# Optimization experiments

Hardware: AMD Instinct MI355X
Metric: run time of the kernel (lower is better)

## Reference

```python
import jax, jax.numpy as jnp
import numpy as np

E, K, N, T, TOPK, GROUP_SIZE = 8, 2048, 2048, 1024, 2, 128


def setup_inputs() -> dict:
    key = jax.random.key(0)
    ks = jax.random.split(key, 6)
    x = jax.random.normal(ks[0], (T, K), dtype=jnp.float32)
    # uint8-quantized weights stored as int32 (values 0..255)
    w_q = jax.random.randint(ks[1], (E, K, N), 0, 256, dtype=jnp.int32)
    scales = jax.random.uniform(ks[2], (E, K, K // GROUP_SIZE), dtype=jnp.float32) * 0.02
    zeros = jax.random.normal(ks[3], (E, K, K // GROUP_SIZE), dtype=jnp.float32) * 0.1
    topk_weights = jax.random.uniform(ks[4], (T, TOPK), dtype=jnp.float32)
    topk_ids = jax.random.randint(ks[5], (T, TOPK), 0, E, dtype=jnp.int32)
    return {"x": x, "w_q": w_q, "scales": scales, "zeros": zeros,
            "topk_weights": topk_weights, "topk_ids": topk_ids}


def reference(x, w_q, scales, zeros, topk_weights, topk_ids):
    # Faithful to _moe_kernel_w8a16: for each (token, expert-slot) pair,
    #   out[t, n] += topk_weight * sum_k x[t, k] * (w_q[e, k, n] * scales[e, k, k//gs] + zeros[e, k, k//gs])
    # Note the kernel broadcasts scale/zero over n (offs_n * 0) with group index k // group_size.
    k_idx = jnp.arange(K)
    g_idx = k_idx // GROUP_SIZE                      # (K,)
    s = scales[:, k_idx, g_idx]                       # (E, K) scale per (e, k)
    z = zeros[:, k_idx, g_idx]                        # (E, K)
    w_deq = w_q.astype(jnp.float32) * s[:, :, None] + z[:, :, None]  # (E, K, N)
    # dense per-expert GEMM, then gather the top_k experts per token
    all_out = jnp.einsum('tk,ekn->ten', x, w_deq)     # (T, E, N)
    sel = jnp.take_along_axis(all_out, topk_ids[:, :, None].astype(jnp.int32), axis=1)  # (T, TOPK, N)
    out = jnp.sum(sel * topk_weights[:, :, None], axis=1)  # (T, N)
    return out
```

## Files before the change

### kernel.cpp

```cpp
#include <hip/hip_runtime.h>
#include <hip/hip_bf16.h>
#include <stdint.h>

#define E_    8
#define K_    2048
#define N_    2048
#define T_    1024
#define TOPK_ 2
#define NG_   16
#define MAXM  512

#define BM 128
#define BN 64
#define BK 64
#define NST (K_ / BK)
#define MTILES (MAXM / BM)

typedef __attribute__((ext_vector_type(8))) short bf16x8;
typedef __attribute__((ext_vector_type(4))) float f32x4;
typedef __attribute__((ext_vector_type(4))) unsigned int u32x4;
typedef __attribute__((ext_vector_type(8))) unsigned short u16x8;

__device__ __forceinline__ unsigned short f2bf_rne(float f) {
    unsigned u = __float_as_uint(f);
    u += 0x7fffu + ((u >> 16) & 1u);
    return (unsigned short)(u >> 16);
}
__device__ __forceinline__ unsigned short f2bf_trunc(float f) {
    return (unsigned short)(__float_as_uint(f) >> 16);
}

__device__ __forceinline__ void gload_lds16(const void* g, void* l) {
    __builtin_amdgcn_global_load_lds(
        (__attribute__((address_space(1))) unsigned int*)g,
        (__attribute__((address_space(3))) unsigned int*)l,
        16, 0, 0);
}

__global__ void prep_sz(const float* __restrict__ scales, const float* __restrict__ zeros,
                        float* __restrict__ sd, float* __restrict__ zd, int* __restrict__ cnt)
{
    int i = blockIdx.x * 256 + threadIdx.x;
    int e = i >> 11;
    int k = i & (K_ - 1);
    int g = k >> 7;
    size_t src = ((size_t)e * K_ + k) * NG_ + g;
    sd[i] = scales[src];
    zd[i] = zeros[src];
    if (i < E_) cnt[i] = 0;
}

__global__ void route_k(const int* __restrict__ topk_ids, int* __restrict__ cnt,
                        int* __restrict__ ptj)
{
    int idx = blockIdx.x * 256 + threadIdx.x;
    if (idx < T_ * TOPK_) {
        int e = topk_ids[idx];
        int slot = atomicAdd(&cnt[e], 1);
        if (slot < T_ * TOPK_) ptj[e * (T_ * TOPK_) + slot] = idx;
    }
}

__global__ void zdot_k(const float* __restrict__ x, const float* __restrict__ zdiag,
                       const int* __restrict__ topk_ids, float* __restrict__ zdot)
{
    int w = (int)((blockIdx.x * blockDim.x + threadIdx.x) >> 6);
    int lane = threadIdx.x & 63;
    int t = w >> 1;
    int e = topk_ids[w];
    const f32x4* xp = (const f32x4*)(x + (size_t)t * K_);
    const f32x4* zp = (const f32x4*)(zdiag + (size_t)e * K_);
    float acc = 0.f;
#pragma unroll
    for (int it = 0; it < K_ / 256; ++it) {
        f32x4 a = xp[it * 64 + lane];
        f32x4 b = zp[it * 64 + lane];
        acc += a.x * b.x + a.y * b.y + a.z * b.z + a.w * b.w;
    }
#pragma unroll
    for (int off = 32; off > 0; off >>= 1) acc += __shfl_xor(acc, off);
    if (lane == 0) zdot[w] = acc;
}

__global__ void aprep_k(const float* __restrict__ x, const float* __restrict__ sdiag,
                        const int* __restrict__ cnt, const int* __restrict__ ptj,
                        unsigned short* __restrict__ apack)
{
    int e = blockIdx.y;
    int slot = blockIdx.x;
    if (slot >= min(cnt[e], MAXM)) return;
    int tj = ptj[e * (T_ * TOPK_) + slot];
    int t = tj >> 1;
    const float* xr = x + (size_t)t * K_;
    const float* sr = sdiag + (size_t)e * K_;
    int k = threadIdx.x * 8;
    f32x4 a0 = *(const f32x4*)(xr + k);
    f32x4 s0 = *(const f32x4*)(sr + k);
    f32x4 a1 = *(const f32x4*)(xr + k + 4);
    f32x4 s1 = *(const f32x4*)(sr + k + 4);
    u16x8 h;
    h[0] = f2bf_rne(a0.x * s0.x);
    h[1] = f2bf_rne(a0.y * s0.y);
    h[2] = f2bf_rne(a0.z * s0.z);
    h[3] = f2bf_rne(a0.w * s0.w);
    h[4] = f2bf_rne(a1.x * s1.x);
    h[5] = f2bf_rne(a1.y * s1.y);
    h[6] = f2bf_rne(a1.z * s1.z);
    h[7] = f2bf_rne(a1.w * s1.w);
    *(u16x8*)(apack + ((size_t)e * MAXM + slot) * K_ + k) = h;
}

__global__ __launch_bounds__(256, 3)
void moe_gemm(const int* __restrict__ wq, const unsigned short* __restrict__ apack,
              const float* __restrict__ topk_w, const int* __restrict__ cnt,
              const int* __restrict__ ptj, const float* __restrict__ zdot,
              float* __restrict__ part, float* __restrict__ out, int use_part)
{
    int e = blockIdx.z;
    int count = min(cnt[e], MAXM);
    int m0 = blockIdx.y * BM;
    if (m0 >= count) return;
    int n0 = blockIdx.x * BN;

    __shared__ alignas(16) unsigned short As[2][BM * BK];
    __shared__ alignas(16) unsigned short Bs[2][BN * BK];

    int tid = threadIdx.x;
    int lane = tid & 63;
    int wid = tid >> 6;
    int wm = (wid >> 1) * 64;
    int wn = (wid & 1) * 32;

    int lrow = lane >> 3;
    int lcol = lane & 7;
    int aswz = (lcol ^ lrow) << 4;
    const char* abase = (const char*)(apack + (size_t)e * MAXM * K_);

    int b_n = tid & 63;
    int b_set = tid >> 6;
    const int* wcol = wq + (size_t)e * K_ * N_ + n0 + b_n;
    int bswz = (b_n & 7) << 4;

    f32x4 acc[4][2] = {};
    int b0[16], b1[16], b2[16];

    auto stageA = [&](int buf, int kt) {
        int kk = kt * BK;
#pragma unroll
        for (int ci = 0; ci < 4; ++ci) {
            int c = wid * 4 + ci;
            int p = m0 + c * 8 + lrow;
            const char* g = abase + ((size_t)p * K_ + kk) * 2 + aswz;
            gload_lds16(g, (char*)As[buf] + c * 1024);
        }
    };
    auto loadB = [&](int* br, int kt) {
        int kb = kt * BK + b_set * 16;
#pragma unroll
        for (int i = 0; i < 16; ++i)
            br[i] = wcol[(kb + i) * N_];
    };
    auto packB = [&](const int* br, int buf) {
        unsigned pk[8];
#pragma unroll
        for (int i = 0; i < 8; ++i) {
            unsigned lo = f2bf_trunc((float)br[2 * i]);
            unsigned hi = f2bf_trunc((float)br[2 * i + 1]);
            pk[i] = lo | (hi << 16);
        }
        char* bsrow = (char*)Bs[buf] + b_n * (BK * 2);
#pragma unroll
        for (int seg = 0; seg < 2; ++seg) {
            int kbyte = b_set * 32 + seg * 16;
            u32x4 v = { pk[seg * 4], pk[seg * 4 + 1], pk[seg * 4 + 2], pk[seg * 4 + 3] };
            *(u32x4*)(bsrow + (kbyte ^ bswz)) = v;
        }
    };
    auto comp = [&](int buf) {
#pragma unroll
        for (int kk2 = 0; kk2 < 2; ++kk2) {
            int kb = kk2 * 64 + ((lane >> 4) << 4);
            bf16x8 af[4], bfr[2];
#pragma unroll
            for (int mi = 0; mi < 4; ++mi) {
                int row = wm + mi * 16 + (lane & 15);
                af[mi] = *(const bf16x8*)((const char*)As[buf] + row * 128 + (kb ^ ((row & 7) << 4)));
            }
#pragma unroll
            for (int ni = 0; ni < 2; ++ni) {
                int row = wn + ni * 16 + (lane & 15);
                bfr[ni] = *(const bf16x8*)((const char*)Bs[buf] + row * 128 + (kb ^ ((row & 7) << 4)));
            }
#pragma unroll
            for (int mi = 0; mi < 4; ++mi)
#pragma unroll
                for (int ni = 0; ni < 2; ++ni)
                    acc[mi][ni] = __builtin_amdgcn_mfma_f32_16x16x32_bf16(
                        af[mi], bfr[ni], acc[mi][ni], 0, 0, 0);
        }
    };

    stageA(0, 0);
    __builtin_amdgcn_sched_barrier(0);
    loadB(b0, 0);
    loadB(b1, 1);
    loadB(b2, 2);
    packB(b0, 0);
    asm volatile("s_waitcnt vmcnt(32) lgkmcnt(0)" ::: "memory");
    __builtin_amdgcn_s_barrier();
    __builtin_amdgcn_sched_barrier(0);

    int kt = 0;
#define STEP(C, BL, BP) do {                                                  \
        stageA(C ^ 1, kt + 1);                                                \
        __builtin_amdgcn_sched_barrier(0);                                    \
        loadB(BL, kt + 3);                                                    \
        comp(C);                                                              \
        packB(BP, C ^ 1);                                                     \
        asm volatile("s_waitcnt vmcnt(16) lgkmcnt(0)" ::: "memory");          \
        __builtin_amdgcn_s_barrier();                                         \
        __builtin_amdgcn_sched_barrier(0);                                    \
        ++kt;                                                                 \
    } while (0)

#pragma unroll 1
    for (int it = 0; it < 4; ++it) {
        STEP(0, b0, b1);
        STEP(1, b1, b2);
        STEP(0, b2, b0);
        STEP(1, b0, b1);
        STEP(0, b1, b2);
        STEP(1, b2, b0);
    }
    STEP(0, b0, b1);
    STEP(1, b1, b2);
    STEP(0, b2, b0);
    STEP(1, b0, b1);
    STEP(0, b1, b2);
#undef STEP
    stageA(0, 30);
    __builtin_amdgcn_sched_barrier(0);
    comp(1);
    packB(b0, 0);
    asm volatile("s_waitcnt vmcnt(0) lgkmcnt(0)" ::: "memory");
    __builtin_amdgcn_s_barrier();
    __builtin_amdgcn_sched_barrier(0);
    stageA(1, 31);
    __builtin_amdgcn_sched_barrier(0);
    comp(0);
    packB(b1, 1);
    asm volatile("s_waitcnt vmcnt(0) lgkmcnt(0)" ::: "memory");
    __builtin_amdgcn_s_barrier();
    __builtin_amdgcn_sched_barrier(0);
    comp(1);

#pragma unroll
    for (int mi = 0; mi < 4; ++mi) {
        int prow = m0 + wm + mi * 16 + ((lane >> 4) << 2);
#pragma unroll
        for (int r = 0; r < 4; ++r) {
            int p = prow + r;
            if (p < count) {
                int tj = ptj[e * (T_ * TOPK_) + p];
                float w = topk_w[tj];
                float zdv = zdot[tj];
                float v0 = w * (acc[mi][0][r] + zdv);
                float v1 = w * (acc[mi][1][r] + zdv);
                if (use_part) {
                    float* pr = part + (size_t)tj * N_ + n0 + wn + (lane & 15);
                    pr[0]  = v0;
                    pr[16] = v1;
                } else {
                    float* orow = out + (size_t)(tj >> 1) * N_ + n0 + wn + (lane & 15);
                    atomicAdd(orow + 0,  v0);
                    atomicAdd(orow + 16, v1);
                }
            }
        }
    }
}

__global__ void reduce_k(const float* __restrict__ part, float* __restrict__ out)
{
    int g = blockIdx.x * 256 + threadIdx.x;
    int t = g >> 9;
    int nc = g & 511;
    f32x4 a = ((const f32x4*)part)[((size_t)(t * 2) << 9) + nc];
    f32x4 b = ((const f32x4*)part)[((size_t)(t * 2 + 1) << 9) + nc];
    ((f32x4*)out)[g] = a + b;
}

extern "C" void kernel_launch(void* const* d_in, const int* in_sizes, int n_in,
                              void* d_out, int out_size, void* d_ws, size_t ws_size,
                              hipStream_t stream)
{
    const float* x       = (const float*)d_in[0];
    const int*   wq      = (const int*)d_in[1];
    const float* scales  = (const float*)d_in[2];
    const float* zeros   = (const float*)d_in[3];
    const float* topk_w  = (const float*)d_in[4];
    const int*   topk_id = (const int*)d_in[5];
    float* out = (float*)d_out;

    char* ws = (char*)d_ws;
    float* sdiag = (float*)(ws + 0);
    float* zdiag = (float*)(ws + 65536);
    int*   cnt   = (int*)(ws + 131072);
    int*   ptj   = (int*)(ws + 135168);
    float* zdot  = (float*)(ws + 200704);
    unsigned short* apack = (unsigned short*)(ws + (1 << 20));
    float* part  = (float*)(ws + ((size_t)17 << 20));
    size_t need = ((size_t)17 << 20) + (size_t)T_ * TOPK_ * N_ * sizeof(float);
    int use_part = (ws_size >= need) ? 1 : 0;

    prep_sz<<<E_ * K_ / 256, 256, 0, stream>>>(scales, zeros, sdiag, zdiag, cnt);
    route_k<<<T_ * TOPK_ / 256, 256, 0, stream>>>(topk_id, cnt, ptj);
    zdot_k<<<T_ * TOPK_ / 4, 256, 0, stream>>>(x, zdiag, topk_id, zdot);
    aprep_k<<<dim3(MAXM, E_), 256, 0, stream>>>(x, sdiag, cnt, ptj, apack);
    if (!use_part)
        hipMemsetAsync(d_out, 0, (size_t)T_ * N_ * sizeof(float), stream);
    moe_gemm<<<dim3(N_ / BN, MTILES, E_), 256, 0, stream>>>(
        wq, apack, topk_w, cnt, ptj, zdot, part, out, use_part);
    if (use_part)
        reduce_k<<<T_ * N_ / 4 / 256, 256, 0, stream>>>(part, out);
}
```

Before: 83.41 us.

## Triple-buffer A tile in LDS to prefetch two k-steps ahead

Adds a third LDS buffer for the activation tile so the direct-to-LDS A loads are issued two k-steps ahead instead of one. The A and B buffer indices are decoupled in the compute routine, and the wait counts are relaxed so more global loads stay in flight. The extra LDS use comes with dropping the occupancy hint from 3 to 2 blocks per CU, which trades latency hiding across blocks for deeper prefetch within a block.

```diff
diff --git a/kernel.cpp b/kernel.cpp
--- a/kernel.cpp
+++ b/kernel.cpp
@@ -110,7 +110,7 @@
     *(u16x8*)(apack + ((size_t)e * MAXM + slot) * K_ + k) = h;
 }
 
-__global__ __launch_bounds__(256, 3)
+__global__ __launch_bounds__(256, 2)
 void moe_gemm(const int* __restrict__ wq, const unsigned short* __restrict__ apack,
               const float* __restrict__ topk_w, const int* __restrict__ cnt,
               const int* __restrict__ ptj, const float* __restrict__ zdot,
@@ -122,7 +122,7 @@
     if (m0 >= count) return;
     int n0 = blockIdx.x * BN;
 
-    __shared__ alignas(16) unsigned short As[2][BM * BK];
+    __shared__ alignas(16) unsigned short As[3][BM * BK];
     __shared__ alignas(16) unsigned short Bs[2][BN * BK];
 
     int tid = threadIdx.x;
@@ -160,7 +160,7 @@
         for (int i = 0; i < 16; ++i)
             br[i] = wcol[(kb + i) * N_];
     };
-    auto packB = [&](const int* br, int buf) {
+    auto packB = [&](const int* br, int bbuf) {
         unsigned pk[8];
 #pragma unroll
         for (int i = 0; i < 8; ++i) {
@@ -168,7 +168,7 @@
             unsigned hi = f2bf_trunc((float)br[2 * i + 1]);
             pk[i] = lo | (hi << 16);
         }
-        char* bsrow = (char*)Bs[buf] + b_n * (BK * 2);
+        char* bsrow = (char*)Bs[bbuf] + b_n * (BK * 2);
 #pragma unroll
         for (int seg = 0; seg < 2; ++seg) {
             int kbyte = b_set * 32 + seg * 16;
@@ -176,7 +176,7 @@
             *(u32x4*)(bsrow + (kbyte ^ bswz)) = v;
         }
     };
-    auto comp = [&](int buf) {
+    auto comp = [&](int abuf, int bbuf) {
 #pragma unroll
         for (int kk2 = 0; kk2 < 2; ++kk2) {
             int kb = kk2 * 64 + ((lane >> 4) << 4);
@@ -184,12 +184,12 @@
 #pragma unroll
             for (int mi = 0; mi < 4; ++mi) {
                 int row = wm + mi * 16 + (lane & 15);
-                af[mi] = *(const bf16x8*)((const char*)As[buf] + row * 128 + (kb ^ ((row & 7) << 4)));
+                af[mi] = *(const bf16x8*)((const char*)As[abuf] + row * 128 + (kb ^ ((row & 7) << 4)));
             }
 #pragma unroll
             for (int ni = 0; ni < 2; ++ni) {
                 int row = wn + ni * 16 + (lane & 15);
-                bfr[ni] = *(const bf16x8*)((const char*)Bs[buf] + row * 128 + (kb ^ ((row & 7) << 4)));
+                bfr[ni] = *(const bf16x8*)((const char*)Bs[bbuf] + row * 128 + (kb ^ ((row & 7) << 4)));
             }
 #pragma unroll
             for (int mi = 0; mi < 4; ++mi)
@@ -201,6 +201,7 @@
     };
 
     stageA(0, 0);
+    stageA(1, 1);
     __builtin_amdgcn_sched_barrier(0);
     loadB(b0, 0);
     loadB(b1, 1);
@@ -211,13 +212,13 @@
     __builtin_amdgcn_sched_barrier(0);
 
     int kt = 0;
-#define STEP(C, BL, BP) do {                                                  \
-        stageA(C ^ 1, kt + 1);                                                \
+#define STEP(CA, SA, BL, BP, CB, PB) do {                                     \
+        stageA(SA, kt + 2);                                                   \
         __builtin_amdgcn_sched_barrier(0);                                    \
         loadB(BL, kt + 3);                                                    \
-        comp(C);                                                              \
-        packB(BP, C ^ 1);                                                     \
-        asm volatile("s_waitcnt vmcnt(16) lgkmcnt(0)" ::: "memory");          \
+        comp(CA, CB);                                                         \
+        packB(BP, PB);                                                        \
+        asm volatile("s_waitcnt vmcnt(36) lgkmcnt(0)" ::: "memory");          \
         __builtin_amdgcn_s_barrier();                                         \
         __builtin_amdgcn_sched_barrier(0);                                    \
         ++kt;                                                                 \
@@ -225,34 +226,32 @@
 
 #pragma unroll 1
     for (int it = 0; it < 4; ++it) {
-        STEP(0, b0, b1);
-        STEP(1, b1, b2);
-        STEP(0, b2, b0);
-        STEP(1, b0, b1);
-        STEP(0, b1, b2);
-        STEP(1, b2, b0);
+        STEP(0, 2, b0, b1, 0, 1);
+        STEP(1, 0, b1, b2, 1, 0);
+        STEP(2, 1, b2, b0, 0, 1);
+        STEP(0, 2, b0, b1, 1, 0);
+        STEP(1, 0, b1, b2, 0, 1);
+        STEP(2, 1, b2, b0, 1, 0);
     }
-    STEP(0, b0, b1);
-    STEP(1, b1, b2);
-    STEP(0, b2, b0);
-    STEP(1, b0, b1);
-    STEP(0, b1, b2);
+    STEP(0, 2, b0, b1, 0, 1);
+    STEP(1, 0, b1, b2, 1, 0);
+    STEP(2, 1, b2, b0, 0, 1);
+    STEP(0, 2, b0, b1, 1, 0);
+    STEP(1, 0, b1, b2, 0, 1);
 #undef STEP
-    stageA(0, 30);
-    __builtin_amdgcn_sched_barrier(0);
-    comp(1);
+    stageA(1, 31);
+    __builtin_amdgcn_sched_barrier(0);
+    comp(2, 1);
     packB(b0, 0);
-    asm volatile("s_waitcnt vmcnt(0) lgkmcnt(0)" ::: "memory");
+    asm volatile("s_waitcnt vmcnt(20) lgkmcnt(0)" ::: "memory");
     __builtin_amdgcn_s_barrier();
     __builtin_amdgcn_sched_barrier(0);
-    stageA(1, 31);
-    __builtin_amdgcn_sched_barrier(0);
-    comp(0);
+    comp(0, 0);
     packB(b1, 1);
     asm volatile("s_waitcnt vmcnt(0) lgkmcnt(0)" ::: "memory");
     __builtin_amdgcn_s_barrier();
     __builtin_amdgcn_sched_barrier(0);
-    comp(1);
+    comp(1, 1);
 
 #pragma unroll
     for (int mi = 0; mi < 4; ++mi) {
```

After: 104.6 us. 1.25x slower.

## Stage A tiles through registers instead of direct global-to-LDS loads

Applied to the files above, without the earlier changes.

Replaces the global_load_lds path for activation tiles with plain vector register loads, two k-steps ahead, followed by swizzled LDS writes after compute. The pipeline is restructured into a uniform 30-step loop and the explicit vmcnt waits and sched_barriers are dropped, leaving vmem waits to the compiler. This gives the compiler more freedom to schedule, at the cost of extra VGPRs for A prefetch and extra LDS write instructions. Loop bounds also change, with B loads clamped at the last tile and redundant loads in the final steps.

```diff
diff --git a/kernel.cpp b/kernel.cpp
--- a/kernel.cpp
+++ b/kernel.cpp
@@ -18,6 +18,7 @@
 
 typedef __attribute__((ext_vector_type(8))) short bf16x8;
 typedef __attribute__((ext_vector_type(4))) float f32x4;
+typedef __attribute__((ext_vector_type(4))) int i32x4;
 typedef __attribute__((ext_vector_type(4))) unsigned int u32x4;
 typedef __attribute__((ext_vector_type(8))) unsigned short u16x8;
 
@@ -28,13 +29,6 @@
 }
 __device__ __forceinline__ unsigned short f2bf_trunc(float f) {
     return (unsigned short)(__float_as_uint(f) >> 16);
-}
-
-__device__ __forceinline__ void gload_lds16(const void* g, void* l) {
-    __builtin_amdgcn_global_load_lds(
-        (__attribute__((address_space(1))) unsigned int*)g,
-        (__attribute__((address_space(3))) unsigned int*)l,
-        16, 0, 0);
 }
 
 __global__ void prep_sz(const float* __restrict__ scales, const float* __restrict__ zeros,
@@ -131,10 +125,11 @@
     int wm = (wid >> 1) * 64;
     int wn = (wid & 1) * 32;
 
-    int lrow = lane >> 3;
-    int lcol = lane & 7;
-    int aswz = (lcol ^ lrow) << 4;
-    const char* abase = (const char*)(apack + (size_t)e * MAXM * K_);
+    int arow = tid >> 3;
+    int asl = tid & 7;
+    const char* ag = (const char*)(apack + (size_t)e * MAXM * K_)
+                   + ((size_t)(m0 + arow) * K_) * 2 + asl * 16;
+    int alds = arow * 128 + ((asl ^ (arow & 7)) << 4);
 
     int b_n = tid & 63;
     int b_set = tid >> 6;
@@ -142,17 +137,20 @@
     int bswz = (b_n & 7) << 4;
 
     f32x4 acc[4][2] = {};
+    i32x4 a0[4], a1[4];
     int b0[16], b1[16], b2[16];
 
-    auto stageA = [&](int buf, int kt) {
-        int kk = kt * BK;
-#pragma unroll
-        for (int ci = 0; ci < 4; ++ci) {
-            int c = wid * 4 + ci;
-            int p = m0 + c * 8 + lrow;
-            const char* g = abase + ((size_t)p * K_ + kk) * 2 + aswz;
-            gload_lds16(g, (char*)As[buf] + c * 1024);
-        }
+    auto loadA = [&](i32x4* dst, int kt) {
+        const char* base = ag + (size_t)kt * (BK * 2);
+#pragma unroll
+        for (int r = 0; r < 4; ++r)
+            dst[r] = *(const i32x4*)(base + (size_t)r * 32 * K_ * 2);
+    };
+    auto writeA = [&](const i32x4* src, int abuf) {
+        char* l = (char*)As[abuf] + alds;
+#pragma unroll
+        for (int r = 0; r < 4; ++r)
+            *(u32x4*)(l + r * 4096) = __builtin_bit_cast(u32x4, src[r]);
     };
     auto loadB = [&](int* br, int kt) {
         int kb = kt * BK + b_set * 16;
@@ -160,7 +158,7 @@
         for (int i = 0; i < 16; ++i)
             br[i] = wcol[(kb + i) * N_];
     };
-    auto packB = [&](const int* br, int buf) {
+    auto packB = [&](const int* br, int bbuf) {
         unsigned pk[8];
 #pragma unroll
         for (int i = 0; i < 8; ++i) {
@@ -168,7 +166,7 @@
             unsigned hi = f2bf_trunc((float)br[2 * i + 1]);
             pk[i] = lo | (hi << 16);
         }
-        char* bsrow = (char*)Bs[buf] + b_n * (BK * 2);
+        char* bsrow = (char*)Bs[bbuf] + b_n * (BK * 2);
 #pragma unroll
         for (int seg = 0; seg < 2; ++seg) {
             int kbyte = b_set * 32 + seg * 16;
@@ -200,58 +198,46 @@
         }
     };
 
-    stageA(0, 0);
-    __builtin_amdgcn_sched_barrier(0);
+    loadA(a0, 0);
+    loadA(a1, 1);
     loadB(b0, 0);
     loadB(b1, 1);
     loadB(b2, 2);
+    writeA(a0, 0);
     packB(b0, 0);
-    asm volatile("s_waitcnt vmcnt(32) lgkmcnt(0)" ::: "memory");
+    asm volatile("s_waitcnt lgkmcnt(0)" ::: "memory");
     __builtin_amdgcn_s_barrier();
-    __builtin_amdgcn_sched_barrier(0);
+    asm volatile("" ::: "memory");
 
     int kt = 0;
-#define STEP(C, BL, BP) do {                                                  \
-        stageA(C ^ 1, kt + 1);                                                \
-        __builtin_amdgcn_sched_barrier(0);                                    \
-        loadB(BL, kt + 3);                                                    \
-        comp(C);                                                              \
-        packB(BP, C ^ 1);                                                     \
-        asm volatile("s_waitcnt vmcnt(16) lgkmcnt(0)" ::: "memory");          \
+#define STEP(AL, BL, CC, AW, BP) do {                                         \
+        loadA(AL, kt + 2);                                                    \
+        loadB(BL, min(kt + 3, NST - 1));                                      \
+        comp(CC);                                                             \
+        writeA(AW, CC ^ 1);                                                   \
+        packB(BP, CC ^ 1);                                                    \
+        asm volatile("s_waitcnt lgkmcnt(0)" ::: "memory");                    \
         __builtin_amdgcn_s_barrier();                                         \
-        __builtin_amdgcn_sched_barrier(0);                                    \
+        asm volatile("" ::: "memory");                                        \
         ++kt;                                                                 \
     } while (0)
 
 #pragma unroll 1
-    for (int it = 0; it < 4; ++it) {
-        STEP(0, b0, b1);
-        STEP(1, b1, b2);
-        STEP(0, b2, b0);
-        STEP(1, b0, b1);
-        STEP(0, b1, b2);
-        STEP(1, b2, b0);
+    for (int it = 0; it < 5; ++it) {
+        STEP(a0, b0, 0, a1, b1);
+        STEP(a1, b1, 1, a0, b2);
+        STEP(a0, b2, 0, a1, b0);
+        STEP(a1, b0, 1, a0, b1);
+        STEP(a0, b1, 0, a1, b2);
+        STEP(a1, b2, 1, a0, b0);
     }
-    STEP(0, b0, b1);
-    STEP(1, b1, b2);
-    STEP(0, b2, b0);
-    STEP(1, b0, b1);
-    STEP(0, b1, b2);
 #undef STEP
-    stageA(0, 30);
-    __builtin_amdgcn_sched_barrier(0);
-    comp(1);
-    packB(b0, 0);
-    asm volatile("s_waitcnt vmcnt(0) lgkmcnt(0)" ::: "memory");
+    comp(0);
+    writeA(a1, 1);
+    packB(b1, 1);
+    asm volatile("s_waitcnt lgkmcnt(0)" ::: "memory");
     __builtin_amdgcn_s_barrier();
-    __builtin_amdgcn_sched_barrier(0);
-    stageA(1, 31);
-    __builtin_amdgcn_sched_barrier(0);
-    comp(0);
-    packB(b1, 1);
-    asm volatile("s_waitcnt vmcnt(0) lgkmcnt(0)" ::: "memory");
-    __builtin_amdgcn_s_barrier();
-    __builtin_amdgcn_sched_barrier(0);
+    asm volatile("" ::: "memory");
     comp(1);
 
 #pragma unroll
```

Result: slower. 90.14 us (+8.1%).

## Double GEMM M-tile to 256 with 512 threads and fuse zero-dot into aprep

Applied to the files above, without the earlier changes.

Raises the GEMM block M-tile from 128 to 256 rows and launches 512 threads per block, so each block reuses every loaded weight column for twice as many tokens. The B loading is redistributed so each thread loads 8 k-rows instead of 16, with the waitcnt values adjusted to match. Separately, the zero-point dot product is computed inside aprep_k, removing one kernel launch and a second read of x. Trade-offs: fewer blocks in flight (MTILES halves) and more shared memory per block, which may reduce occupancy and load balance across experts.

```diff
diff --git a/kernel.cpp b/kernel.cpp
--- a/kernel.cpp
+++ b/kernel.cpp
@@ -10,7 +10,7 @@
 #define NG_   16
 #define MAXM  512
 
-#define BM 128
+#define BM 256
 #define BN 64
 #define BK 64
 #define NST (K_ / BK)
@@ -61,30 +61,10 @@
     }
 }
 
-__global__ void zdot_k(const float* __restrict__ x, const float* __restrict__ zdiag,
-                       const int* __restrict__ topk_ids, float* __restrict__ zdot)
-{
-    int w = (int)((blockIdx.x * blockDim.x + threadIdx.x) >> 6);
-    int lane = threadIdx.x & 63;
-    int t = w >> 1;
-    int e = topk_ids[w];
-    const f32x4* xp = (const f32x4*)(x + (size_t)t * K_);
-    const f32x4* zp = (const f32x4*)(zdiag + (size_t)e * K_);
-    float acc = 0.f;
-#pragma unroll
-    for (int it = 0; it < K_ / 256; ++it) {
-        f32x4 a = xp[it * 64 + lane];
-        f32x4 b = zp[it * 64 + lane];
-        acc += a.x * b.x + a.y * b.y + a.z * b.z + a.w * b.w;
-    }
-#pragma unroll
-    for (int off = 32; off > 0; off >>= 1) acc += __shfl_xor(acc, off);
-    if (lane == 0) zdot[w] = acc;
-}
-
 __global__ void aprep_k(const float* __restrict__ x, const float* __restrict__ sdiag,
+                        const float* __restrict__ zdiag,
                         const int* __restrict__ cnt, const int* __restrict__ ptj,
-                        unsigned short* __restrict__ apack)
+                        unsigned short* __restrict__ apack, float* __restrict__ zdot)
 {
     int e = blockIdx.y;
     int slot = blockIdx.x;
@@ -93,11 +73,14 @@
     int t = tj >> 1;
     const float* xr = x + (size_t)t * K_;
     const float* sr = sdiag + (size_t)e * K_;
+    const float* zr = zdiag + (size_t)e * K_;
     int k = threadIdx.x * 8;
     f32x4 a0 = *(const f32x4*)(xr + k);
     f32x4 s0 = *(const f32x4*)(sr + k);
     f32x4 a1 = *(const f32x4*)(xr + k + 4);
     f32x4 s1 = *(const f32x4*)(sr + k + 4);
+    f32x4 z0 = *(const f32x4*)(zr + k);
+    f32x4 z1 = *(const f32x4*)(zr + k + 4);
     u16x8 h;
     h[0] = f2bf_rne(a0.x * s0.x);
     h[1] = f2bf_rne(a0.y * s0.y);
@@ -108,9 +91,20 @@
     h[6] = f2bf_rne(a1.z * s1.z);
     h[7] = f2bf_rne(a1.w * s1.w);
     *(u16x8*)(apack + ((size_t)e * MAXM + slot) * K_ + k) = h;
-}
-
-__global__ __launch_bounds__(256, 3)
+    float zp = a0.x * z0.x + a0.y * z0.y + a0.z * z0.z + a0.w * z0.w
+             + a1.x * z1.x + a1.y * z1.y + a1.z * z1.z + a1.w * z1.w;
+#pragma unroll
+    for (int off = 32; off > 0; off >>= 1) zp += __shfl_down(zp, off);
+    __shared__ float red[4];
+    int lane = threadIdx.x & 63;
+    int w = threadIdx.x >> 6;
+    if (lane == 0) red[w] = zp;
+    __syncthreads();
+    if (threadIdx.x == 0)
+        zdot[tj] = red[0] + red[1] + red[2] + red[3];
+}
+
+__global__ __launch_bounds__(512, 2)
 void moe_gemm(const int* __restrict__ wq, const unsigned short* __restrict__ apack,
               const float* __restrict__ topk_w, const int* __restrict__ cnt,
               const int* __restrict__ ptj, const float* __restrict__ zdot,
@@ -137,12 +131,12 @@
     const char* abase = (const char*)(apack + (size_t)e * MAXM * K_);
 
     int b_n = tid & 63;
-    int b_set = tid >> 6;
+    int b_kq = tid >> 6;
     const int* wcol = wq + (size_t)e * K_ * N_ + n0 + b_n;
     int bswz = (b_n & 7) << 4;
 
     f32x4 acc[4][2] = {};
-    int b0[16], b1[16], b2[16];
+    int b0[8], b1[8], b2[8];
 
     auto stageA = [&](int buf, int kt) {
         int kk = kt * BK;
@@ -155,26 +149,23 @@
         }
     };
     auto loadB = [&](int* br, int kt) {
-        int kb = kt * BK + b_set * 16;
-#pragma unroll
-        for (int i = 0; i < 16; ++i)
+        int kb = kt * BK + b_kq * 8;
+#pragma unroll
+        for (int i = 0; i < 8; ++i)
             br[i] = wcol[(kb + i) * N_];
     };
-    auto packB = [&](const int* br, int buf) {
-        unsigned pk[8];
-#pragma unroll
-        for (int i = 0; i < 8; ++i) {
+    auto packB = [&](const int* br, int bbuf) {
+        unsigned pk[4];
+#pragma unroll
+        for (int i = 0; i < 4; ++i) {
             unsigned lo = f2bf_trunc((float)br[2 * i]);
             unsigned hi = f2bf_trunc((float)br[2 * i + 1]);
             pk[i] = lo | (hi << 16);
         }
-        char* bsrow = (char*)Bs[buf] + b_n * (BK * 2);
-#pragma unroll
-        for (int seg = 0; seg < 2; ++seg) {
-            int kbyte = b_set * 32 + seg * 16;
-            u32x4 v = { pk[seg * 4], pk[seg * 4 + 1], pk[seg * 4 + 2], pk[seg * 4 + 3] };
-            *(u32x4*)(bsrow + (kbyte ^ bswz)) = v;
-        }
+        char* bsrow = (char*)Bs[bbuf] + b_n * (BK * 2);
+        int kbyte = b_kq * 16;
+        u32x4 v = { pk[0], pk[1], pk[2], pk[3] };
+        *(u32x4*)(bsrow + (kbyte ^ bswz)) = v;
     };
     auto comp = [&](int buf) {
 #pragma unroll
@@ -206,7 +197,7 @@
     loadB(b1, 1);
     loadB(b2, 2);
     packB(b0, 0);
-    asm volatile("s_waitcnt vmcnt(32) lgkmcnt(0)" ::: "memory");
+    asm volatile("s_waitcnt vmcnt(16) lgkmcnt(0)" ::: "memory");
     __builtin_amdgcn_s_barrier();
     __builtin_amdgcn_sched_barrier(0);
 
@@ -217,7 +208,7 @@
         loadB(BL, kt + 3);                                                    \
         comp(C);                                                              \
         packB(BP, C ^ 1);                                                     \
-        asm volatile("s_waitcnt vmcnt(16) lgkmcnt(0)" ::: "memory");          \
+        asm volatile("s_waitcnt vmcnt(8) lgkmcnt(0)" ::: "memory");           \
         __builtin_amdgcn_s_barrier();                                         \
         __builtin_amdgcn_sched_barrier(0);                                    \
         ++kt;                                                                 \
@@ -315,11 +306,10 @@
 
     prep_sz<<<E_ * K_ / 256, 256, 0, stream>>>(scales, zeros, sdiag, zdiag, cnt);
     route_k<<<T_ * TOPK_ / 256, 256, 0, stream>>>(topk_id, cnt, ptj);
-    zdot_k<<<T_ * TOPK_ / 4, 256, 0, stream>>>(x, zdiag, topk_id, zdot);
-    aprep_k<<<dim3(MAXM, E_), 256, 0, stream>>>(x, sdiag, cnt, ptj, apack);
+    aprep_k<<<dim3(MAXM, E_), 256, 0, stream>>>(x, sdiag, zdiag, cnt, ptj, apack, zdot);
     if (!use_part)
         hipMemsetAsync(d_out, 0, (size_t)T_ * N_ * sizeof(float), stream);
-    moe_gemm<<<dim3(N_ / BN, MTILES, E_), 256, 0, stream>>>(
+    moe_gemm<<<dim3(N_ / BN, MTILES, E_), 512, 0, stream>>>(
         wq, apack, topk_w, cnt, ptj, zdot, part, out, use_part);
     if (use_part)
         reduce_k<<<T_ * N_ / 4 / 256, 256, 0, stream>>>(part, out);
```

Measured after the change: 104.2 us. 1.25x slower.
